# Kernel optimization log

Hardware: AMD Instinct MI355X
Metric: run time of the kernel (lower is better)

## Reference

```python
import jax, jax.numpy as jnp
import numpy as np

B, N, F_IN, F_HID, F_LAT = 32, 4096, 128, 64, 32


def setup_inputs() -> dict:
    key = jax.random.key(0)
    ks = jax.random.split(key, 7)
    x = jax.random.normal(ks[0], (B, N, F_IN), dtype=jnp.float32)
    q_ids = jax.random.randint(ks[1], (B,), 0, N)
    # dense (soft) adjacency, as stored on the module
    adj = jax.random.uniform(ks[2], (N, N), dtype=jnp.float32)
    W1 = jax.random.normal(ks[3], (F_IN, F_HID), dtype=jnp.float32) * 0.05
    b1 = jax.random.normal(ks[4], (F_HID,), dtype=jnp.float32) * 0.05
    W2 = jax.random.normal(ks[5], (F_HID, F_LAT), dtype=jnp.float32) * 0.05
    b2 = jax.random.normal(ks[6], (F_LAT,), dtype=jnp.float32) * 0.05
    return {"x": x, "q_ids": q_ids, "adj": adj, "W1": W1, "b1": b1, "W2": W2, "b2": b2}


def reference(x, q_ids, adj, W1, b1, W2, b2):
    # Layer 1 (batched, replaces the per-sample python loop):
    # gcn(x, adj) = adj @ (x @ W1) + b1, then relu
    support = jnp.einsum('bnf,fh->bnh', x, W1)          # (B, N, F_HID)
    h = jax.nn.relu(jnp.einsum('nm,bmh->bnh', adj, support) + b1)
    # Layer 2: each sample uses a single row adj[q_id] -> (1, N) aggregation
    rows = adj[q_ids]                                    # (B, N) gather
    agg = jnp.einsum('bn,bnh->bh', rows, h)              # (B, F_HID)
    out = agg @ W2 + b2                                  # (B, F_LAT), squeezed
    return out
```

## Files before the change

### kernel.cpp

```cpp
#include <hip/hip_runtime.h>
#include <hip/hip_bf16.h>
#include <stdint.h>

typedef __attribute__((ext_vector_type(4))) float f32x4;
typedef __attribute__((ext_vector_type(8))) short short8;

#define NN 4096
#define FIN 128
#define FHID 64
#define BATCH 32
#define NJ 2048

__device__ __forceinline__ unsigned short f2bf(float f) {
  unsigned u = __builtin_bit_cast(unsigned, f);
  u = (u + 0x7FFFu + ((u >> 16) & 1u)) >> 16;
  return (unsigned short)u;
}
__device__ __forceinline__ float bf2f(unsigned short h) {
  unsigned u = ((unsigned)h) << 16;
  return __builtin_bit_cast(float, u);
}
__device__ __forceinline__ void gload_lds16(const void* g, void* l) {
  __builtin_amdgcn_global_load_lds(
      (const __attribute__((address_space(1))) unsigned int*)g,
      (__attribute__((address_space(3))) unsigned int*)l, 16, 0, 0);
}

__global__ __launch_bounds__(256) void k_pre(const float* __restrict__ adj,
                                             unsigned short* __restrict__ adjb,
                                             const float* __restrict__ x,
                                             const float* __restrict__ W1,
                                             unsigned short* __restrict__ St) {
  __shared__ unsigned short W1t[FHID * 136];
  __shared__ __align__(16) unsigned short T[FHID * 128];
  const int tid = threadIdx.x;

  if (blockIdx.x >= 1024) {
    long base = ((long)blockIdx.x - 1024) * 2048 + tid;
    const f32x4* in = (const f32x4*)adj;
    f32x4 v[8];
    #pragma unroll
    for (int it = 0; it < 8; ++it) v[it] = in[base + it * 256];
    #pragma unroll
    for (int it = 0; it < 8; ++it) {
      ushort4 o;
      o.x = f2bf(v[it].x); o.y = f2bf(v[it].y);
      o.z = f2bf(v[it].z); o.w = f2bf(v[it].w);
      *(ushort4*)(adjb + (base + it * 256) * 4) = o;
    }
    return;
  }

  for (int i = tid; i < FIN * FHID; i += 256) {
    int f = i >> 6, h = i & 63;
    W1t[h * 136 + f] = f2bf(W1[i]);
  }
  __syncthreads();

  const int bb = blockIdx.x >> 5;
  const int m0 = (blockIdx.x & 31) * 128;
  const int lane = tid & 63, wv = tid >> 6;
  const int fr = lane & 15, fq = lane >> 4;

  short8 bfr[4][4];
  #pragma unroll
  for (int ni = 0; ni < 4; ++ni)
    #pragma unroll
    for (int ks = 0; ks < 4; ++ks)
      bfr[ni][ks] = *(const short8*)&W1t[(ni * 16 + fr) * 136 + ks * 32 + fq * 8];

  const float* xr0 = x + ((size_t)bb * NN + m0 + wv * 32 + fr) * FIN;
  const float* xr1 = xr0 + (size_t)16 * FIN;

  f32x4 z = {0.f, 0.f, 0.f, 0.f};
  f32x4 acc[2][4];
  #pragma unroll
  for (int mf = 0; mf < 2; ++mf)
    #pragma unroll
    for (int ni = 0; ni < 4; ++ni) acc[mf][ni] = z;

  #pragma unroll
  for (int ks = 0; ks < 4; ++ks) {
    #pragma unroll
    for (int mf = 0; mf < 2; ++mf) {
      const float* src = (mf ? xr1 : xr0) + ks * 32 + fq * 8;
      f32x4 lo = *(const f32x4*)src;
      f32x4 hi = *(const f32x4*)(src + 4);
      short8 a;
      #pragma unroll
      for (int j = 0; j < 4; ++j) { a[j] = (short)f2bf(lo[j]); a[4 + j] = (short)f2bf(hi[j]); }
      #pragma unroll
      for (int ni = 0; ni < 4; ++ni)
        acc[mf][ni] = __builtin_amdgcn_mfma_f32_16x16x32_bf16(a, bfr[ni][ks], acc[mf][ni], 0, 0, 0);
    }
  }

  const int cr = (lane >> 4) * 4, cc = lane & 15;
  #pragma unroll
  for (int mf = 0; mf < 2; ++mf)
    #pragma unroll
    for (int ni = 0; ni < 4; ++ni) {
      ushort4 o;
      o.x = f2bf(acc[mf][ni][0]); o.y = f2bf(acc[mf][ni][1]);
      o.z = f2bf(acc[mf][ni][2]); o.w = f2bf(acc[mf][ni][3]);
      *(ushort4*)&T[(ni * 16 + cc) * 128 + wv * 32 + mf * 16 + cr] = o;
    }
  __syncthreads();
  for (int u = tid; u < FHID * 16; u += 256) {
    int row = u >> 4, ch = u & 15;
    *(short8*)(St + (size_t)(bb * FHID + row) * NN + m0 + ch * 8) =
        *(const short8*)&T[row * 128 + ch * 8];
  }
}

#define VMW(N)  asm volatile("s_waitcnt vmcnt(" #N ")" ::: "memory")
#define LGKM0   asm volatile("s_waitcnt lgkmcnt(0)" ::: "memory")
#define BAR     __builtin_amdgcn_s_barrier()

__global__ __launch_bounds__(512, 1) void k_gemm(const unsigned short* __restrict__ A,
                                                 const unsigned short* __restrict__ Bt,
                                                 const float* __restrict__ b1,
                                                 const float* __restrict__ adj,
                                                 const int* __restrict__ q_ids,
                                                 float* __restrict__ partial) {
  __shared__ __align__(16) unsigned short As[2 * 16384];
  __shared__ __align__(16) unsigned short Bs[2 * 8192];
  __shared__ float adjw[2][256];
  __shared__ float red[8][64];

  const int tid  = threadIdx.x;
  const int lane = tid & 63;
  const int wv   = tid >> 6;
  const int wm   = wv >> 1;
  const int wn   = wv & 1;
  const int bm   = blockIdx.x * 256;
  const int bn   = blockIdx.y * 128;
  const int fr   = lane & 15;
  const int fq   = lane >> 4;

  int offA[2][2][2], offB[4][2];
  #pragma unroll
  for (int h = 0; h < 2; ++h)
    #pragma unroll
    for (int m2 = 0; m2 < 2; ++m2) {
      int row = wm * 32 + h * 128 + m2 * 16 + fr;
      #pragma unroll
      for (int ks = 0; ks < 2; ++ks)
        offA[h][m2][ks] = row * 64 + ((((ks << 6) + (fq << 4)) ^ ((row & 7) << 4)) >> 1);
    }
  #pragma unroll
  for (int ni = 0; ni < 4; ++ni) {
    int row = wn * 32 + (ni & 1) * 16 + (ni >> 1) * 64 + fr;
    #pragma unroll
    for (int ks = 0; ks < 2; ++ks)
      offB[ni][ks] = row * 64 + ((((ks << 6) + (fq << 4)) ^ ((row & 7) << 4)) >> 1);
  }

  const int srow = tid >> 3;
  const int scol = ((((tid & 7) << 4) ^ ((srow & 7) << 4)) >> 1);
  const unsigned short* gA00 = A + (size_t)(bm +   0 + srow) * NN + scol;
  const unsigned short* gA01 = A + (size_t)(bm +  64 + srow) * NN + scol;
  const unsigned short* gA10 = A + (size_t)(bm + 128 + srow) * NN + scol;
  const unsigned short* gA11 = A + (size_t)(bm + 192 + srow) * NN + scol;
  const unsigned short* gB0  = Bt + (size_t)(bn +  0 + srow) * NN + scol;
  const unsigned short* gB1  = Bt + (size_t)(bn + 64 + srow) * NN + scol;
  const int ld = tid * 8;

  f32x4 z = {0.f, 0.f, 0.f, 0.f};
  f32x4 acc[4][4];
  #pragma unroll
  for (int i = 0; i < 4; ++i)
    #pragma unroll
    for (int j = 0; j < 4; ++j) acc[i][j] = z;

  short8 av0[2][2], av1[2][2], bv0[2][2], bv1[2][2];

#define RD_AVA(Ac)                                                             \
    _Pragma("unroll") for (int m2 = 0; m2 < 2; ++m2)                           \
    _Pragma("unroll") for (int ks = 0; ks < 2; ++ks)                           \
      av0[m2][ks] = *(const short8*)((Ac) + offA[0][m2][ks]);
#define RD_AVB(Ac)                                                             \
    _Pragma("unroll") for (int m2 = 0; m2 < 2; ++m2)                           \
    _Pragma("unroll") for (int ks = 0; ks < 2; ++ks)                           \
      av1[m2][ks] = *(const short8*)((Ac) + offA[1][m2][ks]);
#define RD_BV(DST, Bb, P)                                                      \
    _Pragma("unroll") for (int n2 = 0; n2 < 2; ++n2)                           \
    _Pragma("unroll") for (int ks = 0; ks < 2; ++ks)                           \
      DST[n2][ks] = *(const short8*)((Bb) + offB[2 * (P) + n2][ks]);
#define MFMA8(MP, AV, BV, NP)                                                  \
    __builtin_amdgcn_s_setprio(1);                                             \
    _Pragma("unroll") for (int m2 = 0; m2 < 2; ++m2)                           \
    _Pragma("unroll") for (int n2 = 0; n2 < 2; ++n2)                           \
    _Pragma("unroll") for (int ks = 0; ks < 2; ++ks)                           \
      acc[2 * (MP) + m2][2 * (NP) + n2] = __builtin_amdgcn_mfma_f32_16x16x32_bf16( \
          AV[m2][ks], BV[n2][ks], acc[2 * (MP) + m2][2 * (NP) + n2], 0, 0, 0); \
    __builtin_amdgcn_s_setprio(0);

#define TILE(CUR, KOA, KOB, DOSA, DOSB, VMWA, VMWB) {                          \
    const unsigned short* Ac = As + (CUR) * 16384;                             \
    const unsigned short* Bc = Bs + (CUR) * 8192;                              \
                                                                      \
    RD_AVA(Ac)                                                                 \
    RD_BV(bv0, Bc, 0)                                                          \
    RD_BV(bv1, Bc, 1)                                                          \
    VMWA;                                                                      \
    if (DOSA) {         \
      gload_lds16(gA10 + (KOA), As + (1 - (CUR)) * 16384 + 2 * 4096 + ld);     \
      gload_lds16(gA11 + (KOA), As + (1 - (CUR)) * 16384 + 3 * 4096 + ld);     \
    }                                                                          \
    BAR; LGKM0;                                                                \
    MFMA8(0, av0, bv0, 0)                                                      \
    MFMA8(0, av0, bv1, 1)                                                      \
                                                                      \
    RD_AVB(Ac)                                                                 \
    VMWB;                                                                      \
    if (DOSB) {    \
      gload_lds16(gA00 + (KOB), As + (CUR) * 16384 + 0 * 4096 + ld);           \
      gload_lds16(gA01 + (KOB), As + (CUR) * 16384 + 1 * 4096 + ld);           \
      gload_lds16(gB0  + (KOB), Bs + (CUR) * 8192 + 0 * 4096 + ld);            \
      gload_lds16(gB1  + (KOB), Bs + (CUR) * 8192 + 1 * 4096 + ld);            \
    }                                                                          \
    BAR; LGKM0;                                                                \
    MFMA8(1, av1, bv1, 1)                                                      \
    MFMA8(1, av1, bv0, 0)                                                      \
  }

  gload_lds16(gA00,      As + 0 * 4096 + ld);
  gload_lds16(gA01,      As + 1 * 4096 + ld);
  gload_lds16(gB0,       Bs + 0 * 4096 + ld);
  gload_lds16(gB1,       Bs + 1 * 4096 + ld);
  gload_lds16(gA10,      As + 2 * 4096 + ld);
  gload_lds16(gA11,      As + 3 * 4096 + ld);
  gload_lds16(gA00 + 64, As + 16384 + 0 * 4096 + ld);
  gload_lds16(gA01 + 64, As + 16384 + 1 * 4096 + ld);
  gload_lds16(gB0  + 64, Bs + 8192 + 0 * 4096 + ld);
  gload_lds16(gB1  + 64, Bs + 8192 + 1 * 4096 + ld);
  VMW(4);
  BAR;

  int koa = 64;
  int kob = 128;
  #pragma unroll 1
  for (int g = 0; g < 31; ++g) {
    TILE(0, koa,      kob,      1, 1, VMW(6), VMW(6))
    TILE(1, koa + 64, kob + 64, 1, 1, VMW(6), VMW(6))
    koa += 128; kob += 128;
  }
  TILE(0, 63 * 64, 0, 1, 0, VMW(6), VMW(6))
  TILE(1, 0, 0, 0, 0, VMW(2), VMW(0))
#undef RD_AVA
#undef RD_AVB
#undef RD_BV
#undef MFMA8
#undef TILE

  const int b0 = bn >> 6;
  {
    int bsel = tid >> 8;
    int rloc = tid & 255;
    adjw[bsel][rloc] = adj[(size_t)q_ids[b0 + bsel] * NN + bm + rloc];
  }
  __syncthreads();

  const int cr = (lane >> 4) * 4;
  const int cc = lane & 15;
  float ps[4];
  #pragma unroll
  for (int ni = 0; ni < 4; ++ni) {
    int colh = wn * 32 + (ni & 1) * 16 + cc;
    float bias = b1[colh];
    float s = 0.f;
    #pragma unroll
    for (int mi = 0; mi < 4; ++mi) {
      int rowl = wm * 32 + (mi & 1) * 16 + (mi >> 1) * 128 + cr;
      #pragma unroll
      for (int r = 0; r < 4; ++r) {
        float v = acc[mi][ni][r] + bias;
        v = v > 0.f ? v : 0.f;
        s += adjw[ni >> 1][rowl + r] * v;
      }
    }
    ps[ni] = s;
  }
  #pragma unroll
  for (int ni = 0; ni < 4; ++ni) {
    ps[ni] += __shfl_xor(ps[ni], 16, 64);
    ps[ni] += __shfl_xor(ps[ni], 32, 64);
  }
  if (lane < 16) {
    #pragma unroll
    for (int ni = 0; ni < 4; ++ni)
      red[wm * 2 + wn][ni * 16 + cc] = ps[ni];
  }
  __syncthreads();
  if (tid < 128) {
    int colLocal = tid;
    int wn2 = (colLocal >> 5) & 1;
    int ni2 = ((colLocal >> 6) << 1) | ((colLocal >> 4) & 1);
    int cc2 = colLocal & 15;
    float s = red[0 + wn2][ni2 * 16 + cc2] + red[2 + wn2][ni2 * 16 + cc2]
            + red[4 + wn2][ni2 * 16 + cc2] + red[6 + wn2][ni2 * 16 + cc2];
    partial[(size_t)blockIdx.x * NJ + bn + colLocal] = s;
  }
}

__global__ __launch_bounds__(1024) void k_out(const float* __restrict__ partial,
                                              const float* __restrict__ W2,
                                              const float* __restrict__ b2,
                                              float* __restrict__ out) {
  __shared__ float aggs[BATCH * FHID];
  int t = threadIdx.x;
  for (int idx = t; idx < BATCH * FHID; idx += 1024) {
    float s = 0.f;
    #pragma unroll
    for (int c = 0; c < 16; ++c) s += partial[c * NJ + idx];
    aggs[idx] = s;
  }
  __syncthreads();
  int b = t >> 5, l = t & 31;
  float o = b2[l];
  #pragma unroll
  for (int h = 0; h < FHID; ++h) o += aggs[b * FHID + h] * W2[h * 32 + l];
  out[b * 32 + l] = o;
}

extern "C" void kernel_launch(void* const* d_in, const int* in_sizes, int n_in,
                              void* d_out, int out_size, void* d_ws, size_t ws_size,
                              hipStream_t stream) {
  const float* x   = (const float*)d_in[0];
  const int*   q   = (const int*)d_in[1];
  const float* adj = (const float*)d_in[2];
  const float* W1  = (const float*)d_in[3];
  const float* b1  = (const float*)d_in[4];
  const float* W2  = (const float*)d_in[5];
  const float* b2  = (const float*)d_in[6];
  float* out = (float*)d_out;

  char* ws = (char*)d_ws;
  unsigned short* adjb   = (unsigned short*)ws;
  unsigned short* St     = (unsigned short*)(ws + (size_t)32 * 1024 * 1024);
  float*          partial= (float*)(ws + (size_t)48 * 1024 * 1024);

  k_pre<<<3072, 256, 0, stream>>>(adj, adjb, x, W1, St);
  dim3 g2(NN / 256, NJ / 128);
  k_gemm<<<g2, 512, 0, stream>>>(adjb, St, b1, adj, q, partial);
  k_out<<<1, 1024, 0, stream>>>(partial, W2, b2, out);
}
```

Before: 94.76 us.

## Load B fragments directly from global into registers, bypassing LDS

```diff
diff --git a/kernel.cpp b/kernel.cpp
--- a/kernel.cpp
+++ b/kernel.cpp
@@ -124,7 +124,6 @@
                                                  const int* __restrict__ q_ids,
                                                  float* __restrict__ partial) {
   __shared__ __align__(16) unsigned short As[2 * 16384];
-  __shared__ __align__(16) unsigned short Bs[2 * 8192];
   __shared__ float adjw[2][256];
   __shared__ float red[8][64];
 
@@ -138,7 +137,7 @@
   const int fr   = lane & 15;
   const int fq   = lane >> 4;
 
-  int offA[2][2][2], offB[4][2];
+  int offA[2][2][2];
   #pragma unroll
   for (int h = 0; h < 2; ++h)
     #pragma unroll
@@ -148,13 +147,14 @@
       for (int ks = 0; ks < 2; ++ks)
         offA[h][m2][ks] = row * 64 + ((((ks << 6) + (fq << 4)) ^ ((row & 7) << 4)) >> 1);
     }
-  #pragma unroll
-  for (int ni = 0; ni < 4; ++ni) {
-    int row = wn * 32 + (ni & 1) * 16 + (ni >> 1) * 64 + fr;
+
+  const unsigned short* gBF[4][2];
+  #pragma unroll
+  for (int j = 0; j < 4; ++j)
     #pragma unroll
     for (int ks = 0; ks < 2; ++ks)
-      offB[ni][ks] = row * 64 + ((((ks << 6) + (fq << 4)) ^ ((row & 7) << 4)) >> 1);
-  }
+      gBF[j][ks] = Bt + (size_t)(bn + wn * 32 + (j & 1) * 16 + (j >> 1) * 64 + fr) * NN
+                   + fq * 8 + ks * 32;
 
   const int srow = tid >> 3;
   const int scol = ((((tid & 7) << 4) ^ ((srow & 7) << 4)) >> 1);
@@ -162,8 +162,6 @@
   const unsigned short* gA01 = A + (size_t)(bm +  64 + srow) * NN + scol;
   const unsigned short* gA10 = A + (size_t)(bm + 128 + srow) * NN + scol;
   const unsigned short* gA11 = A + (size_t)(bm + 192 + srow) * NN + scol;
-  const unsigned short* gB0  = Bt + (size_t)(bn +  0 + srow) * NN + scol;
-  const unsigned short* gB1  = Bt + (size_t)(bn + 64 + srow) * NN + scol;
   const int ld = tid * 8;
 
   f32x4 z = {0.f, 0.f, 0.f, 0.f};
@@ -173,7 +171,7 @@
     #pragma unroll
     for (int j = 0; j < 4; ++j) acc[i][j] = z;
 
-  short8 av0[2][2], av1[2][2], bv0[2][2], bv1[2][2];
+  short8 av0[2][2], av1[2][2], bvE[4][2], bvO[4][2];
 
 #define RD_AVA(Ac)                                                             \
     _Pragma("unroll") for (int m2 = 0; m2 < 2; ++m2)                           \
@@ -183,74 +181,66 @@
     _Pragma("unroll") for (int m2 = 0; m2 < 2; ++m2)                           \
     _Pragma("unroll") for (int ks = 0; ks < 2; ++ks)                           \
       av1[m2][ks] = *(const short8*)((Ac) + offA[1][m2][ks]);
-#define RD_BV(DST, Bb, P)                                                      \
-    _Pragma("unroll") for (int n2 = 0; n2 < 2; ++n2)                           \
+#define LOAD_B8(DST, KQ)                                                       \
+    _Pragma("unroll") for (int j = 0; j < 4; ++j)                              \
     _Pragma("unroll") for (int ks = 0; ks < 2; ++ks)                           \
-      DST[n2][ks] = *(const short8*)((Bb) + offB[2 * (P) + n2][ks]);
+      DST[j][ks] = *(const short8*)(gBF[j][ks] + (KQ));
 #define MFMA8(MP, AV, BV, NP)                                                  \
     __builtin_amdgcn_s_setprio(1);                                             \
     _Pragma("unroll") for (int m2 = 0; m2 < 2; ++m2)                           \
     _Pragma("unroll") for (int n2 = 0; n2 < 2; ++n2)                           \
     _Pragma("unroll") for (int ks = 0; ks < 2; ++ks)                           \
       acc[2 * (MP) + m2][2 * (NP) + n2] = __builtin_amdgcn_mfma_f32_16x16x32_bf16( \
-          AV[m2][ks], BV[n2][ks], acc[2 * (MP) + m2][2 * (NP) + n2], 0, 0, 0); \
+          AV[m2][ks], BV[2 * (NP) + n2][ks], acc[2 * (MP) + m2][2 * (NP) + n2], 0, 0, 0); \
     __builtin_amdgcn_s_setprio(0);
 
-#define TILE(CUR, KOA, KOB, DOSA, DOSB, VMWA, VMWB) {                          \
+#define TILE(CUR, BVC, BVN, KN1, KN2, DOB8, DOSA, DOSB, VMWA, VMWB) {          \
     const unsigned short* Ac = As + (CUR) * 16384;                             \
-    const unsigned short* Bc = Bs + (CUR) * 8192;                              \
                                                                       \
     RD_AVA(Ac)                                                                 \
-    RD_BV(bv0, Bc, 0)                                                          \
-    RD_BV(bv1, Bc, 1)                                                          \
+    if (DOB8) { LOAD_B8(BVN, KN1) }                                            \
+    if (DOSA) {             \
+      gload_lds16(gA10 + (KN1), As + (1 - (CUR)) * 16384 + 2 * 4096 + ld);     \
+      gload_lds16(gA11 + (KN1), As + (1 - (CUR)) * 16384 + 3 * 4096 + ld);     \
+    }                                                                          \
     VMWA;                                                                      \
-    if (DOSA) {         \
-      gload_lds16(gA10 + (KOA), As + (1 - (CUR)) * 16384 + 2 * 4096 + ld);     \
-      gload_lds16(gA11 + (KOA), As + (1 - (CUR)) * 16384 + 3 * 4096 + ld);     \
-    }                                                                          \
     BAR; LGKM0;                                                                \
-    MFMA8(0, av0, bv0, 0)                                                      \
-    MFMA8(0, av0, bv1, 1)                                                      \
+    MFMA8(0, av0, BVC, 0)                                                      \
+    MFMA8(0, av0, BVC, 1)                                                      \
                                                                       \
     RD_AVB(Ac)                                                                 \
+    if (DOSB) {         \
+      gload_lds16(gA00 + (KN2), As + (CUR) * 16384 + 0 * 4096 + ld);           \
+      gload_lds16(gA01 + (KN2), As + (CUR) * 16384 + 1 * 4096 + ld);           \
+    }                                                                          \
     VMWB;                                                                      \
-    if (DOSB) {    \
-      gload_lds16(gA00 + (KOB), As + (CUR) * 16384 + 0 * 4096 + ld);           \
-      gload_lds16(gA01 + (KOB), As + (CUR) * 16384 + 1 * 4096 + ld);           \
-      gload_lds16(gB0  + (KOB), Bs + (CUR) * 8192 + 0 * 4096 + ld);            \
-      gload_lds16(gB1  + (KOB), Bs + (CUR) * 8192 + 1 * 4096 + ld);            \
-    }                                                                          \
     BAR; LGKM0;                                                                \
-    MFMA8(1, av1, bv1, 1)                                                      \
-    MFMA8(1, av1, bv0, 0)                                                      \
-  }
-
+    MFMA8(1, av1, BVC, 1)                                                      \
+    MFMA8(1, av1, BVC, 0)                                                      \
+  }
+
+  LOAD_B8(bvE, 0)
   gload_lds16(gA00,      As + 0 * 4096 + ld);
   gload_lds16(gA01,      As + 1 * 4096 + ld);
-  gload_lds16(gB0,       Bs + 0 * 4096 + ld);
-  gload_lds16(gB1,       Bs + 1 * 4096 + ld);
   gload_lds16(gA10,      As + 2 * 4096 + ld);
   gload_lds16(gA11,      As + 3 * 4096 + ld);
   gload_lds16(gA00 + 64, As + 16384 + 0 * 4096 + ld);
   gload_lds16(gA01 + 64, As + 16384 + 1 * 4096 + ld);
-  gload_lds16(gB0  + 64, Bs + 8192 + 0 * 4096 + ld);
-  gload_lds16(gB1  + 64, Bs + 8192 + 1 * 4096 + ld);
-  VMW(4);
+  VMW(2);
   BAR;
 
-  int koa = 64;
-  int kob = 128;
+  int kn = 0;
   #pragma unroll 1
   for (int g = 0; g < 31; ++g) {
-    TILE(0, koa,      kob,      1, 1, VMW(6), VMW(6))
-    TILE(1, koa + 64, kob + 64, 1, 1, VMW(6), VMW(6))
-    koa += 128; kob += 128;
-  }
-  TILE(0, 63 * 64, 0, 1, 0, VMW(6), VMW(6))
-  TILE(1, 0, 0, 0, 0, VMW(2), VMW(0))
+    TILE(0, bvE, bvO, kn +  64, kn + 128, 1, 1, 1, VMW(12), VMW(12))
+    TILE(1, bvO, bvE, kn + 128, kn + 192, 1, 1, 1, VMW(12), VMW(12))
+    kn += 128;
+  }
+  TILE(0, bvE, bvO, 62 * 64 + 64, 0, 1, 1, 0, VMW(12), VMW(10))
+  TILE(1, bvO, bvE, 0, 0, 0, 0, 0, VMW(0), (void)0)
 #undef RD_AVA
 #undef RD_AVB
-#undef RD_BV
+#undef LOAD_B8
 #undef MFMA8
 #undef TILE
 
```

New measurement: 189.4 us. 2x slower.
